# Kernel optimization log

Hardware: AMD Instinct MI355X
Metric: run time of the kernel (lower is better)

Reference implementation:

```python
import jax, jax.numpy as jnp
import numpy as np

N = 50000   # nodes
C = 64      # channels (in == out)
E = 800000  # edges (before self-loops)
EPS = 1e-5  # BatchNorm eps


def _bn(h, gamma, beta):
    # training-mode BatchNorm1d over the node (batch) axis
    mu = h.mean(0)
    var = h.var(0)
    return (h - mu) * jax.lax.rsqrt(var + EPS) * gamma + beta


def setup_inputs() -> dict:
    key = jax.random.key(0)
    ks = jax.random.split(key, 20)
    p = lambda i, shape, s=0.1: jax.random.normal(ks[i], shape, jnp.float32) * s
    src = jax.random.randint(ks[2], (E,), 0, N, dtype=jnp.int32)
    # guarantee no self-loops (PointTransformerConv removes then re-adds them)
    dst = (src + 1 + jax.random.randint(ks[3], (E,), 0, N - 1, dtype=jnp.int32)) % N
    return dict(
        x=p(0, (N, C), 1.0),
        pos=p(1, (N, 3), 1.0),
        edge_index=jnp.stack([src, dst]),
        Win=p(4, (C, C)), bin_=p(5, (C,)), gin=jnp.ones((C,), jnp.float32), betain=jnp.zeros((C,), jnp.float32),
        Wv=p(6, (C, C)), Wk=p(7, (C, C)), Wq=p(8, (C, C)),
        P1=p(9, (3, C)), pb1=p(10, (C,)), P2=p(11, (C, C)), pb2=p(12, (C,)),
        A1=p(13, (C, C)), ab1=p(14, (C,)), A2=p(15, (C, C)), ab2=p(16, (C,)),
        Wout=p(17, (C, C)), bout=p(18, (C,)), gout=jnp.ones((C,), jnp.float32), betaout=jnp.zeros((C,), jnp.float32),
    )


def reference(x, pos, edge_index, Win, bin_, gin, betain, Wv, Wk, Wq,
              P1, pb1, P2, pb2, A1, ab1, A2, ab2, Wout, bout, gout, betaout):
    silu = jax.nn.silu
    # mlp_in: Linear + BN + SiLU (plain_last=False)
    x = silu(_bn(x @ Win + bin_, gin, betain))

    # PointTransformerConv (add_self_loops=True)
    loop = jnp.arange(N, dtype=edge_index.dtype)
    src = jnp.concatenate([edge_index[0], loop])  # j
    dst = jnp.concatenate([edge_index[1], loop])  # i

    v = x @ Wv       # lin (values), bias=False
    k = x @ Wk       # lin_src
    q = x @ Wq       # lin_dst

    # per-edge positional encoding: pos_nn = SiLU(SiLU((pos_i - pos_j) P1 + b) P2 + b)
    delta = silu(silu((pos[dst] - pos[src]) @ P1 + pb1) @ P2 + pb2)  # [Etot, C]
    # attention logits: attn_nn(alpha_i - alpha_j + delta)
    alpha = q[dst] - k[src] + delta
    alpha = silu(silu(alpha @ A1 + ab1) @ A2 + ab2)

    # segment-wise (per-dst-node, per-channel) softmax over neighborhoods
    m = jax.ops.segment_max(alpha, dst, num_segments=N)
    ex = jnp.exp(alpha - m[dst])
    denom = jax.ops.segment_sum(ex, dst, num_segments=N)
    attn = ex / denom[dst]

    # weighted scatter-reduce of messages
    out = jax.ops.segment_sum(attn * (v[src] + delta), dst, num_segments=N)  # [N, C]

    # mlp_out: Linear + BN, act=None
    return _bn(out @ Wout + bout, gout, betaout)
```

## Files before the change

### kernel.cpp

```cpp
#include <hip/hip_runtime.h>

#define CH 64
#define BN_EPS 1e-5f

typedef __attribute__((ext_vector_type(8))) __bf16 bf16x8;
typedef __attribute__((ext_vector_type(4))) __bf16 bf16x4;
typedef __attribute__((ext_vector_type(4))) float f32x4;

__device__ __forceinline__ float silu_f(float x) { return x / (1.0f + __expf(-x)); }

__global__ __launch_bounds__(256) void k_lin_in(
    const float* __restrict__ x, const float* __restrict__ Win, const float* __restrict__ bin,
    float* __restrict__ h, float* __restrict__ ssum, float* __restrict__ ssq, int N)
{
    __shared__ float xt[64 * 64];
    __shared__ float Wl[64 * 64];
    __shared__ float red[2][4][64];
    const int t = threadIdx.x, c = t & 63, g = t >> 6;
    const int row0 = blockIdx.x * 64;

    for (int i = t; i < 64 * 64; i += 256) {
        int r = i >> 6, cc = i & 63;
        int gr = row0 + r;
        xt[i] = (gr < N) ? x[(size_t)gr * CH + cc] : 0.0f;
        Wl[i] = Win[i];
    }
    __syncthreads();

    float acc[16];
    const float b = bin[c];
#pragma unroll
    for (int i = 0; i < 16; ++i) acc[i] = b;
    for (int k = 0; k < 64; ++k) {
        float w = Wl[k * 64 + c];
#pragma unroll
        for (int i = 0; i < 16; ++i) acc[i] += xt[(g * 16 + i) * 64 + k] * w;
    }
    float s = 0.0f, ss = 0.0f;
#pragma unroll
    for (int i = 0; i < 16; ++i) {
        int gr = row0 + g * 16 + i;
        if (gr < N) {
            h[(size_t)gr * CH + c] = acc[i];
            s += acc[i];
            ss += acc[i] * acc[i];
        }
    }
    red[0][g][c] = s;
    red[1][g][c] = ss;
    __syncthreads();
    if (g == 0) {
        atomicAdd(&ssum[c], red[0][0][c] + red[0][1][c] + red[0][2][c] + red[0][3][c]);
        atomicAdd(&ssq[c],  red[1][0][c] + red[1][1][c] + red[1][2][c] + red[1][3][c]);
    }
}

__global__ void k_stats(const float* __restrict__ ssum, const float* __restrict__ ssq,
                        const float* __restrict__ gamma, const float* __restrict__ beta,
                        float* __restrict__ scale, float* __restrict__ shift, int N)
{
    int c = threadIdx.x;
    float inv = 1.0f / (float)N;
    float mu = ssum[c] * inv;
    float var = ssq[c] * inv - mu * mu;
    float sc = gamma[c] * rsqrtf(var + BN_EPS);
    scale[c] = sc;
    shift[c] = beta[c] - mu * sc;
}

__global__ __launch_bounds__(256) void k_vkq(
    const float* __restrict__ h, const float* __restrict__ scale, const float* __restrict__ shift,
    const float* __restrict__ Wv, const float* __restrict__ Wk, const float* __restrict__ Wq,
    __bf16* __restrict__ vv, __bf16* __restrict__ kk, __bf16* __restrict__ qq, int N)
{
    __shared__ float xt[64 * 64];
    __shared__ float Wl[2][64 * 64];
    const int t = threadIdx.x, c = t & 63, g = t >> 6;
    const int row0 = blockIdx.x * 64;

    for (int i = t; i < 64 * 64; i += 256) {
        int r = i >> 6, cc = i & 63;
        int gr = row0 + r;
        float hv = (gr < N) ? h[(size_t)gr * CH + cc] : 0.0f;
        xt[i] = silu_f(hv * scale[cc] + shift[cc]);
        Wl[0][i] = Wv[i];
        Wl[1][i] = Wk[i];
    }
    __syncthreads();

    for (int m = 0; m < 2; ++m) {
        float acc[16];
#pragma unroll
        for (int i = 0; i < 16; ++i) acc[i] = 0.0f;
        for (int k = 0; k < 64; ++k) {
            float w = Wl[m][k * 64 + c];
#pragma unroll
            for (int i = 0; i < 16; ++i) acc[i] += xt[(g * 16 + i) * 64 + k] * w;
        }
        __bf16* o = (m == 0) ? vv : kk;
#pragma unroll
        for (int i = 0; i < 16; ++i) {
            int gr = row0 + g * 16 + i;
            if (gr < N) o[(size_t)gr * CH + c] = (__bf16)acc[i];
        }
    }
    __syncthreads();
    for (int i = t; i < 64 * 64; i += 256) Wl[0][i] = Wq[i];
    __syncthreads();
    {
        float acc[16];
#pragma unroll
        for (int i = 0; i < 16; ++i) acc[i] = 0.0f;
        for (int k = 0; k < 64; ++k) {
            float w = Wl[0][k * 64 + c];
#pragma unroll
            for (int i = 0; i < 16; ++i) acc[i] += xt[(g * 16 + i) * 64 + k] * w;
        }
#pragma unroll
        for (int i = 0; i < 16; ++i) {
            int gr = row0 + g * 16 + i;
            if (gr < N) qq[(size_t)gr * CH + c] = (__bf16)acc[i];
        }
    }
}

__global__ __launch_bounds__(256, 2) void k_edge_mfma(
    const int* __restrict__ srcA, const int* __restrict__ dstA,
    const float* __restrict__ pos,
    const __bf16* __restrict__ vvb, const __bf16* __restrict__ kkb, const __bf16* __restrict__ qqb,
    const float* __restrict__ P1, const float* __restrict__ pb1,
    const float* __restrict__ P2, const float* __restrict__ pb2,
    const float* __restrict__ A1, const float* __restrict__ ab1,
    const float* __restrict__ A2, const float* __restrict__ ab2,
    float* __restrict__ num, float* __restrict__ den,
    int E, int Etot, int nChunks)
{
    __shared__ __align__(16) __bf16 Wtab[3][8][64][8];
    __shared__ __align__(16) __bf16 tb[4][16][66];
    __shared__ __align__(16) __bf16 P1L[3][64];
    __shared__ __align__(16) float pb1L[64];

    const int t = threadIdx.x;
    for (int i = t; i < 3 * 4096; i += 256) {
        int mat = i >> 12, r = i & 4095;
        int j = r & 7, lane = (r >> 3) & 63, ksnt = r >> 9;
        int ks = ksnt & 1, nt = ksnt >> 1;
        int k = ks * 32 + ((lane >> 4) & 3) * 8 + j;
        int n = nt * 16 + (lane & 15);
        const float* W = (mat == 0) ? P2 : ((mat == 1) ? A1 : A2);
        Wtab[mat][ksnt][lane][j] = (__bf16)W[k * 64 + n];
    }
    if (t < 192) P1L[t / 64][t & 63] = (__bf16)P1[t];
    if (t < 64)  pb1L[t] = pb1[t];
    __syncthreads();

    const int l = t & 63, wid = t >> 6, lg = l >> 4, lm = l & 15;
    __bf16* tbw = &tb[wid][0][0];

    float pb2r[4], ab1r[4], ab2r[4];
#pragma unroll
    for (int nt = 0; nt < 4; ++nt) {
        int co = nt * 16 + lm;
        pb2r[nt] = pb2[co];
        ab1r[nt] = ab1[co]; ab2r[nt] = ab2[co];
    }

    const int stride = gridDim.x;
    int ch = blockIdx.x;
    if (ch >= nChunks) return;

    int sC = 0, dC = 0;
    {
        int eA = ch * 64 + wid * 16 + lm;
        if (eA < Etot) { if (eA < E) { sC = srcA[eA]; dC = dstA[eA]; } else { sC = dC = eA - E; } }
    }
    float pdl0, pdl1, pdl2;
    bf16x8 qmk0, qmk1;
    {
        const float* ps = pos + (size_t)sC * 3;
        const float* pd = pos + (size_t)dC * 3;
        pdl0 = pd[0] - ps[0]; pdl1 = pd[1] - ps[1]; pdl2 = pd[2] - ps[2];
        const __bf16* qp = qqb + (size_t)dC * 64 + lg * 8;
        const __bf16* kp = kkb + (size_t)sC * 64 + lg * 8;
        bf16x8 q0 = *(const bf16x8*)qp, q1 = *(const bf16x8*)(qp + 32);
        bf16x8 k0 = *(const bf16x8*)kp, k1 = *(const bf16x8*)(kp + 32);
#pragma unroll
        for (int j = 0; j < 8; ++j) {
            qmk0[j] = (__bf16)((float)q0[j] - (float)k0[j]);
            qmk1[j] = (__bf16)((float)q1[j] - (float)k1[j]);
        }
    }
    __bf16 vcur[4][4];
#pragma unroll
    for (int jj = 0; jj < 4; ++jj) {
        int sD = __shfl(sC, lg * 4 + jj);
        const __bf16* vp = vvb + (size_t)sD * 64 + lm;
#pragma unroll
        for (int nt = 0; nt < 4; ++nt) vcur[jj][nt] = vp[nt * 16];
    }
    int chn = ch + stride;
    bool hn = chn < nChunks;
    int sN = 0, dN = 0;
    if (hn) {
        int eA = chn * 64 + wid * 16 + lm;
        if (eA < Etot) { if (eA < E) { sN = srcA[eA]; dN = dstA[eA]; } else { sN = dN = eA - E; } }
    }

    for (;;) {
        const int e0 = ch * 64 + wid * 16;

        bf16x8 aX0, aX1;
#pragma unroll
        for (int f = 0; f < 2; ++f) {
            const int k0 = f * 32 + lg * 8;
            bf16x8 w0 = *(const bf16x8*)&P1L[0][k0];
            bf16x8 w1 = *(const bf16x8*)&P1L[1][k0];
            bf16x8 w2 = *(const bf16x8*)&P1L[2][k0];
            f32x4 b0 = *(const f32x4*)&pb1L[k0];
            f32x4 b1 = *(const f32x4*)&pb1L[k0 + 4];
#pragma unroll
            for (int j = 0; j < 8; ++j) {
                float bb = (j < 4) ? b0[j & 3] : b1[j & 3];
                float tv = silu_f(pdl0 * (float)w0[j] + pdl1 * (float)w1[j] +
                                  pdl2 * (float)w2[j] + bb);
                if (f == 0) aX0[j] = (__bf16)tv; else aX1[j] = (__bf16)tv;
            }
        }

        f32x4 acc[4];
#pragma unroll
        for (int nt = 0; nt < 4; ++nt) {
            f32x4 a; a[0] = a[1] = a[2] = a[3] = pb2r[nt];
            a = __builtin_amdgcn_mfma_f32_16x16x32_bf16(aX0, *(const bf16x8*)&Wtab[0][nt * 2 + 0][l][0], a, 0, 0, 0);
            a = __builtin_amdgcn_mfma_f32_16x16x32_bf16(aX1, *(const bf16x8*)&Wtab[0][nt * 2 + 1][l][0], a, 0, 0, 0);
            acc[nt] = a;
        }
        bf16x4 dltb[4];
#pragma unroll
        for (int nt = 0; nt < 4; ++nt)
#pragma unroll
            for (int jj = 0; jj < 4; ++jj) {
                float dv = silu_f(acc[nt][jj]);
                dltb[nt][jj] = (__bf16)dv;
                tbw[(lg * 4 + jj) * 66 + nt * 16 + lm] = (__bf16)dv;
            }

        float pdlN0 = 0.f, pdlN1 = 0.f, pdlN2 = 0.f;
        bf16x8 qmkN0, qmkN1;
        __bf16 vN[4][4];
        if (hn) {
            const float* ps = pos + (size_t)sN * 3;
            const float* pd = pos + (size_t)dN * 3;
            pdlN0 = pd[0] - ps[0]; pdlN1 = pd[1] - ps[1]; pdlN2 = pd[2] - ps[2];
            const __bf16* qp = qqb + (size_t)dN * 64 + lg * 8;
            const __bf16* kp = kkb + (size_t)sN * 64 + lg * 8;
            bf16x8 q0 = *(const bf16x8*)qp, q1 = *(const bf16x8*)(qp + 32);
            bf16x8 k0 = *(const bf16x8*)kp, k1 = *(const bf16x8*)(kp + 32);
#pragma unroll
            for (int j = 0; j < 8; ++j) {
                qmkN0[j] = (__bf16)((float)q0[j] - (float)k0[j]);
                qmkN1[j] = (__bf16)((float)q1[j] - (float)k1[j]);
            }
#pragma unroll
            for (int jj = 0; jj < 4; ++jj) {
                int sD = __shfl(sN, lg * 4 + jj);
                const __bf16* vp = vvb + (size_t)sD * 64 + lm;
#pragma unroll
                for (int nt = 0; nt < 4; ++nt) vN[jj][nt] = vp[nt * 16];
            }
        }

        const int chn2 = chn + stride;
        const bool hn2 = hn && (chn2 < nChunks);
        int sNN = 0, dNN = 0;
        if (hn2) {
            int eA = chn2 * 64 + wid * 16 + lm;
            if (eA < Etot) { if (eA < E) { sNN = srcA[eA]; dNN = dstA[eA]; } else { sNN = dNN = eA - E; } }
        }

        bf16x8 dA0 = *(const bf16x8*)&tbw[lm * 66 + lg * 8];
        bf16x8 dA1 = *(const bf16x8*)&tbw[lm * 66 + 32 + lg * 8];
        bf16x8 aA0, aA1;
#pragma unroll
        for (int j = 0; j < 8; ++j) {
            aA0[j] = (__bf16)((float)qmk0[j] + (float)dA0[j]);
            aA1[j] = (__bf16)((float)qmk1[j] + (float)dA1[j]);
        }

#pragma unroll
        for (int nt = 0; nt < 4; ++nt) {
            f32x4 a; a[0] = a[1] = a[2] = a[3] = ab1r[nt];
            a = __builtin_amdgcn_mfma_f32_16x16x32_bf16(aA0, *(const bf16x8*)&Wtab[1][nt * 2 + 0][l][0], a, 0, 0, 0);
            a = __builtin_amdgcn_mfma_f32_16x16x32_bf16(aA1, *(const bf16x8*)&Wtab[1][nt * 2 + 1][l][0], a, 0, 0, 0);
            acc[nt] = a;
        }
#pragma unroll
        for (int nt = 0; nt < 4; ++nt)
#pragma unroll
            for (int jj = 0; jj < 4; ++jj)
                tbw[(lg * 4 + jj) * 66 + nt * 16 + lm] = (__bf16)silu_f(acc[nt][jj]);
        bf16x8 aY0 = *(const bf16x8*)&tbw[lm * 66 + lg * 8];
        bf16x8 aY1 = *(const bf16x8*)&tbw[lm * 66 + 32 + lg * 8];

#pragma unroll
        for (int nt = 0; nt < 4; ++nt) {
            f32x4 a; a[0] = a[1] = a[2] = a[3] = ab2r[nt];
            a = __builtin_amdgcn_mfma_f32_16x16x32_bf16(aY0, *(const bf16x8*)&Wtab[2][nt * 2 + 0][l][0], a, 0, 0, 0);
            a = __builtin_amdgcn_mfma_f32_16x16x32_bf16(aY1, *(const bf16x8*)&Wtab[2][nt * 2 + 1][l][0], a, 0, 0, 0);
            acc[nt] = a;
        }

#pragma unroll
        for (int jj = 0; jj < 4; ++jj) {
            const int eD = e0 + lg * 4 + jj;
            const bool v = eD < Etot;
            const int dD = __shfl(dC, lg * 4 + jj);
            const size_t ob = (size_t)dD * 64 + lm;
#pragma unroll
            for (int nt = 0; nt < 4; ++nt) {
                float ex = v ? __expf(silu_f(acc[nt][jj])) : 0.0f;
                atomicAdd(&den[ob + nt * 16], ex);
                atomicAdd(&num[ob + nt * 16], ex * ((float)vcur[jj][nt] + (float)dltb[nt][jj]));
            }
        }

        if (!hn) break;
        ch = chn; chn = chn2; hn = hn2;
        sC = sN; dC = dN; sN = sNN; dN = dNN;
        pdl0 = pdlN0; pdl1 = pdlN1; pdl2 = pdlN2;
        qmk0 = qmkN0; qmk1 = qmkN1;
#pragma unroll
        for (int jj = 0; jj < 4; ++jj)
#pragma unroll
            for (int nt = 0; nt < 4; ++nt) vcur[jj][nt] = vN[jj][nt];
    }
}

__global__ __launch_bounds__(256) void k_out(
    const float* __restrict__ num, const float* __restrict__ den,
    const float* __restrict__ Wout, const float* __restrict__ bout,
    float* __restrict__ o, float* __restrict__ ssum, float* __restrict__ ssq, int N)
{
    __shared__ float xt[64 * 64];
    __shared__ float Wl[64 * 64];
    __shared__ float red[2][4][64];
    const int t = threadIdx.x, c = t & 63, g = t >> 6;
    const int row0 = blockIdx.x * 64;

    for (int i = t; i < 64 * 64; i += 256) {
        int r = i >> 6, cc = i & 63;
        int gr = row0 + r;
        xt[i] = (gr < N) ? num[(size_t)gr * CH + cc] / den[(size_t)gr * CH + cc] : 0.0f;
        Wl[i] = Wout[i];
    }
    __syncthreads();

    float acc[16];
    const float b = bout[c];
#pragma unroll
    for (int i = 0; i < 16; ++i) acc[i] = b;
    for (int k = 0; k < 64; ++k) {
        float w = Wl[k * 64 + c];
#pragma unroll
        for (int i = 0; i < 16; ++i) acc[i] += xt[(g * 16 + i) * 64 + k] * w;
    }
    float s = 0.0f, ss = 0.0f;
#pragma unroll
    for (int i = 0; i < 16; ++i) {
        int gr = row0 + g * 16 + i;
        if (gr < N) {
            o[(size_t)gr * CH + c] = acc[i];
            s += acc[i];
            ss += acc[i] * acc[i];
        }
    }
    red[0][g][c] = s;
    red[1][g][c] = ss;
    __syncthreads();
    if (g == 0) {
        atomicAdd(&ssum[c], red[0][0][c] + red[0][1][c] + red[0][2][c] + red[0][3][c]);
        atomicAdd(&ssq[c],  red[1][0][c] + red[1][1][c] + red[1][2][c] + red[1][3][c]);
    }
}

__global__ void k_final(const float* __restrict__ o, const float* __restrict__ scale,
                        const float* __restrict__ shift, float* __restrict__ out, int total)
{
    int i = blockIdx.x * blockDim.x + threadIdx.x;
    if (i < total) {
        int c = i & 63;
        out[i] = o[i] * scale[c] + shift[c];
    }
}

extern "C" void kernel_launch(void* const* d_in, const int* in_sizes, int n_in,
                              void* d_out, int out_size, void* d_ws, size_t ws_size,
                              hipStream_t stream)
{
    const float* x      = (const float*)d_in[0];
    const float* pos    = (const float*)d_in[1];
    const int*   ei     = (const int*)d_in[2];
    const float* Win    = (const float*)d_in[3];
    const float* bin    = (const float*)d_in[4];
    const float* gin    = (const float*)d_in[5];
    const float* betain = (const float*)d_in[6];
    const float* Wv     = (const float*)d_in[7];
    const float* Wk     = (const float*)d_in[8];
    const float* Wq     = (const float*)d_in[9];
    const float* P1     = (const float*)d_in[10];
    const float* pb1    = (const float*)d_in[11];
    const float* P2     = (const float*)d_in[12];
    const float* pb2    = (const float*)d_in[13];
    const float* A1     = (const float*)d_in[14];
    const float* ab1    = (const float*)d_in[15];
    const float* A2     = (const float*)d_in[16];
    const float* ab2    = (const float*)d_in[17];
    const float* Wout   = (const float*)d_in[18];
    const float* bout   = (const float*)d_in[19];
    const float* gout   = (const float*)d_in[20];
    const float* betaout= (const float*)d_in[21];

    const int N = in_sizes[0] / CH;
    const int E = in_sizes[2] / 2;
    const int Etot = E + N;
    const int* srcA = ei;
    const int* dstA = ei + E;

    float* ws = (float*)d_ws;
    const size_t NC = (size_t)N * CH;
    float* h    = ws;
    float* num  = h + NC;
    float* den  = num + NC;
    float* st   = den + NC;
    __bf16* vvb = (__bf16*)(st + 512);
    __bf16* kkb = vvb + NC;
    __bf16* qqb = kkb + NC;

    hipMemsetAsync(num, 0, (2 * NC + 512) * sizeof(float), stream);

    const int nb = (N + 63) / 64;
    k_lin_in<<<nb, 256, 0, stream>>>(x, Win, bin, h, st, st + 64, N);
    k_stats<<<1, 64, 0, stream>>>(st, st + 64, gin, betain, st + 128, st + 192, N);
    k_vkq<<<nb, 256, 0, stream>>>(h, st + 128, st + 192, Wv, Wk, Wq, vvb, kkb, qqb, N);

    const int nChunks = (Etot + 63) / 64;
    const int grid = (nChunks < 1024) ? nChunks : 1024;
    k_edge_mfma<<<grid, 256, 0, stream>>>(srcA, dstA, pos, vvb, kkb, qqb,
                                          P1, pb1, P2, pb2, A1, ab1, A2, ab2,
                                          num, den, E, Etot, nChunks);

    k_out<<<nb, 256, 0, stream>>>(num, den, Wout, bout, h, st + 256, st + 320, N);
    k_stats<<<1, 64, 0, stream>>>(st + 256, st + 320, gout, betaout, st + 384, st + 448, N);
    k_final<<<(int)((NC + 255) / 256), 256, 0, stream>>>(h, st + 384, st + 448,
                                                         (float*)d_out, (int)NC);
}
```

Measured before the change: 565.9 us.

## Sort edges by destination (CSR) and reduce per-node in shared memory

Builds a CSR ordering of edges by destination each call, using a histogram, a three-stage scan and an atomic scatter. The edge kernel then assigns 8 destination nodes per block, accumulates softmax numerator and denominator with shared-memory atomics, and writes the normalized result directly. This removes the global float atomics on num/den and the separate division, but adds several sorting kernels and drops the software prefetch pipeline along with the persistent grid. Blocks that get many edges become load-imbalanced, and launching roughly 6250 blocks means reloading the weight tables into shared memory in every block.

```diff
diff --git a/kernel.cpp b/kernel.cpp
--- a/kernel.cpp
+++ b/kernel.cpp
@@ -2,6 +2,7 @@
 
 #define CH 64
 #define BN_EPS 1e-5f
+#define DPB 8
 
 typedef __attribute__((ext_vector_type(8))) __bf16 bf16x8;
 typedef __attribute__((ext_vector_type(4))) __bf16 bf16x4;
@@ -124,21 +125,97 @@
     }
 }
 
-__global__ __launch_bounds__(256, 2) void k_edge_mfma(
-    const int* __restrict__ srcA, const int* __restrict__ dstA,
+__global__ void k_hist(const int* __restrict__ dstA, int* __restrict__ cnt, int E, int Etot)
+{
+    int e = blockIdx.x * blockDim.x + threadIdx.x;
+    if (e < Etot) {
+        int d = (e < E) ? dstA[e] : (e - E);
+        atomicAdd(&cnt[d], 1);
+    }
+}
+
+__global__ __launch_bounds__(256) void k_scan_a(
+    const int* __restrict__ cnt, int* __restrict__ exc, int* __restrict__ bsum, int N)
+{
+    __shared__ int sh[256];
+    const int b = blockIdx.x, t = threadIdx.x;
+    const int base = b * 1024 + t * 4;
+    int v0 = (base + 0 < N) ? cnt[base + 0] : 0;
+    int v1 = (base + 1 < N) ? cnt[base + 1] : 0;
+    int v2 = (base + 2 < N) ? cnt[base + 2] : 0;
+    int v3 = (base + 3 < N) ? cnt[base + 3] : 0;
+    int s = v0 + v1 + v2 + v3;
+    sh[t] = s;
+    __syncthreads();
+    for (int off = 1; off < 256; off <<= 1) {
+        int x = (t >= off) ? sh[t - off] : 0;
+        __syncthreads();
+        sh[t] += x;
+        __syncthreads();
+    }
+    int p = sh[t] - s;
+    if (t == 255) bsum[b] = sh[255];
+    if (base + 0 < N) exc[base + 0] = p; p += v0;
+    if (base + 1 < N) exc[base + 1] = p; p += v1;
+    if (base + 2 < N) exc[base + 2] = p; p += v2;
+    if (base + 3 < N) exc[base + 3] = p;
+}
+
+__global__ __launch_bounds__(256) void k_scan_b(int* __restrict__ bsum, int nb)
+{
+    __shared__ int sh[256];
+    const int t = threadIdx.x;
+    int v = (t < nb) ? bsum[t] : 0;
+    sh[t] = v;
+    __syncthreads();
+    for (int off = 1; off < 256; off <<= 1) {
+        int x = (t >= off) ? sh[t - off] : 0;
+        __syncthreads();
+        sh[t] += x;
+        __syncthreads();
+    }
+    if (t < nb) bsum[t] = sh[t] - v;
+}
+
+__global__ void k_scan_c(const int* __restrict__ exc, const int* __restrict__ bsum,
+                         int* __restrict__ rowptr, int* __restrict__ cur, int N)
+{
+    int i = blockIdx.x * blockDim.x + threadIdx.x;
+    if (i < N) {
+        int r = exc[i] + bsum[i >> 10];
+        rowptr[i] = r;
+        cur[i] = r;
+    }
+}
+
+__global__ void k_scatter(const int* __restrict__ srcA, const int* __restrict__ dstA,
+                          int* __restrict__ cur, int2* __restrict__ sortedSD, int E, int Etot)
+{
+    int e = blockIdx.x * blockDim.x + threadIdx.x;
+    if (e < Etot) {
+        int d, s;
+        if (e < E) { d = dstA[e]; s = srcA[e]; }
+        else       { d = s = e - E; }
+        int p = atomicAdd(&cur[d], 1);
+        sortedSD[p] = make_int2(s, d);
+    }
+}
+
+__global__ __launch_bounds__(256) void k_edge_grp(
+    const int2* __restrict__ sortedSD, const int* __restrict__ rowptr,
     const float* __restrict__ pos,
     const __bf16* __restrict__ vvb, const __bf16* __restrict__ kkb, const __bf16* __restrict__ qqb,
     const float* __restrict__ P1, const float* __restrict__ pb1,
     const float* __restrict__ P2, const float* __restrict__ pb2,
     const float* __restrict__ A1, const float* __restrict__ ab1,
     const float* __restrict__ A2, const float* __restrict__ ab2,
-    float* __restrict__ num, float* __restrict__ den,
-    int E, int Etot, int nChunks)
+    float* __restrict__ pre, int N, int Etot)
 {
     __shared__ __align__(16) __bf16 Wtab[3][8][64][8];
     __shared__ __align__(16) __bf16 tb[4][16][66];
     __shared__ __align__(16) __bf16 P1L[3][64];
     __shared__ __align__(16) float pb1L[64];
+    __shared__ float accS[2][DPB][64];
 
     const int t = threadIdx.x;
     for (int i = t; i < 3 * 4096; i += 256) {
@@ -152,6 +229,8 @@
     }
     if (t < 192) P1L[t / 64][t & 63] = (__bf16)P1[t];
     if (t < 64)  pb1L[t] = pb1[t];
+#pragma unroll
+    for (int i = t; i < 2 * DPB * 64; i += 256) ((float*)accS)[i] = 0.0f;
     __syncthreads();
 
     const int l = t & 63, wid = t >> 6, lg = l >> 4, lm = l & 15;
@@ -165,59 +244,55 @@
         ab1r[nt] = ab1[co]; ab2r[nt] = ab2[co];
     }
 
-    const int stride = gridDim.x;
-    int ch = blockIdx.x;
-    if (ch >= nChunks) return;
-
-    int sC = 0, dC = 0;
-    {
-        int eA = ch * 64 + wid * 16 + lm;
-        if (eA < Etot) { if (eA < E) { sC = srcA[eA]; dC = dstA[eA]; } else { sC = dC = eA - E; } }
-    }
-    float pdl0, pdl1, pdl2;
-    bf16x8 qmk0, qmk1;
-    {
+    const int D0 = blockIdx.x * DPB;
+    const int R0 = rowptr[D0];
+    const int R1 = (D0 + DPB >= N) ? Etot : rowptr[D0 + DPB];
+    const int nE = R1 - R0;
+
+    for (int win = wid; win * 16 < nE; win += 4) {
+        const int eBase = R0 + win * 16;
+        const int eA = eBase + lm;
+        int sC = 0, dloc = 0;
+        int dC = D0;
+        if (eA < R1) {
+            int2 sd = sortedSD[eA];
+            sC = sd.x; dC = sd.y;
+            dloc = dC - D0;
+        }
+
         const float* ps = pos + (size_t)sC * 3;
         const float* pd = pos + (size_t)dC * 3;
-        pdl0 = pd[0] - ps[0]; pdl1 = pd[1] - ps[1]; pdl2 = pd[2] - ps[2];
+        float pdl0 = pd[0] - ps[0], pdl1 = pd[1] - ps[1], pdl2 = pd[2] - ps[2];
         const __bf16* qp = qqb + (size_t)dC * 64 + lg * 8;
         const __bf16* kp = kkb + (size_t)sC * 64 + lg * 8;
         bf16x8 q0 = *(const bf16x8*)qp, q1 = *(const bf16x8*)(qp + 32);
         bf16x8 k0 = *(const bf16x8*)kp, k1 = *(const bf16x8*)(kp + 32);
+        bf16x8 qmk0, qmk1;
 #pragma unroll
         for (int j = 0; j < 8; ++j) {
             qmk0[j] = (__bf16)((float)q0[j] - (float)k0[j]);
             qmk1[j] = (__bf16)((float)q1[j] - (float)k1[j]);
         }
-    }
-    __bf16 vcur[4][4];
-#pragma unroll
-    for (int jj = 0; jj < 4; ++jj) {
-        int sD = __shfl(sC, lg * 4 + jj);
-        const __bf16* vp = vvb + (size_t)sD * 64 + lm;
-#pragma unroll
-        for (int nt = 0; nt < 4; ++nt) vcur[jj][nt] = vp[nt * 16];
-    }
-    int chn = ch + stride;
-    bool hn = chn < nChunks;
-    int sN = 0, dN = 0;
-    if (hn) {
-        int eA = chn * 64 + wid * 16 + lm;
-        if (eA < Etot) { if (eA < E) { sN = srcA[eA]; dN = dstA[eA]; } else { sN = dN = eA - E; } }
-    }
-
-    for (;;) {
-        const int e0 = ch * 64 + wid * 16;
+        int dlocD[4];
+        __bf16 vcur[4][4];
+#pragma unroll
+        for (int jj = 0; jj < 4; ++jj) {
+            int sD = __shfl(sC, lg * 4 + jj);
+            dlocD[jj] = __shfl(dloc, lg * 4 + jj);
+            const __bf16* vp = vvb + (size_t)sD * 64 + lm;
+#pragma unroll
+            for (int nt = 0; nt < 4; ++nt) vcur[jj][nt] = vp[nt * 16];
+        }
 
         bf16x8 aX0, aX1;
 #pragma unroll
         for (int f = 0; f < 2; ++f) {
-            const int k0 = f * 32 + lg * 8;
-            bf16x8 w0 = *(const bf16x8*)&P1L[0][k0];
-            bf16x8 w1 = *(const bf16x8*)&P1L[1][k0];
-            bf16x8 w2 = *(const bf16x8*)&P1L[2][k0];
-            f32x4 b0 = *(const f32x4*)&pb1L[k0];
-            f32x4 b1 = *(const f32x4*)&pb1L[k0 + 4];
+            const int k0i = f * 32 + lg * 8;
+            bf16x8 w0 = *(const bf16x8*)&P1L[0][k0i];
+            bf16x8 w1 = *(const bf16x8*)&P1L[1][k0i];
+            bf16x8 w2 = *(const bf16x8*)&P1L[2][k0i];
+            f32x4 b0 = *(const f32x4*)&pb1L[k0i];
+            f32x4 b1 = *(const f32x4*)&pb1L[k0i + 4];
 #pragma unroll
             for (int j = 0; j < 8; ++j) {
                 float bb = (j < 4) ? b0[j & 3] : b1[j & 3];
@@ -245,39 +320,6 @@
                 tbw[(lg * 4 + jj) * 66 + nt * 16 + lm] = (__bf16)dv;
             }
 
-        float pdlN0 = 0.f, pdlN1 = 0.f, pdlN2 = 0.f;
-        bf16x8 qmkN0, qmkN1;
-        __bf16 vN[4][4];
-        if (hn) {
-            const float* ps = pos + (size_t)sN * 3;
-            const float* pd = pos + (size_t)dN * 3;
-            pdlN0 = pd[0] - ps[0]; pdlN1 = pd[1] - ps[1]; pdlN2 = pd[2] - ps[2];
-            const __bf16* qp = qqb + (size_t)dN * 64 + lg * 8;
-            const __bf16* kp = kkb + (size_t)sN * 64 + lg * 8;
-            bf16x8 q0 = *(const bf16x8*)qp, q1 = *(const bf16x8*)(qp + 32);
-            bf16x8 k0 = *(const bf16x8*)kp, k1 = *(const bf16x8*)(kp + 32);
-#pragma unroll
-            for (int j = 0; j < 8; ++j) {
-                qmkN0[j] = (__bf16)((float)q0[j] - (float)k0[j]);
-                qmkN1[j] = (__bf16)((float)q1[j] - (float)k1[j]);
-            }
-#pragma unroll
-            for (int jj = 0; jj < 4; ++jj) {
-                int sD = __shfl(sN, lg * 4 + jj);
-                const __bf16* vp = vvb + (size_t)sD * 64 + lm;
-#pragma unroll
-                for (int nt = 0; nt < 4; ++nt) vN[jj][nt] = vp[nt * 16];
-            }
-        }
-
-        const int chn2 = chn + stride;
-        const bool hn2 = hn && (chn2 < nChunks);
-        int sNN = 0, dNN = 0;
-        if (hn2) {
-            int eA = chn2 * 64 + wid * 16 + lm;
-            if (eA < Etot) { if (eA < E) { sNN = srcA[eA]; dNN = dstA[eA]; } else { sNN = dNN = eA - E; } }
-        }
-
         bf16x8 dA0 = *(const bf16x8*)&tbw[lm * 66 + lg * 8];
         bf16x8 dA1 = *(const bf16x8*)&tbw[lm * 66 + 32 + lg * 8];
         bf16x8 aA0, aA1;
@@ -312,32 +354,32 @@
 
 #pragma unroll
         for (int jj = 0; jj < 4; ++jj) {
-            const int eD = e0 + lg * 4 + jj;
-            const bool v = eD < Etot;
-            const int dD = __shfl(dC, lg * 4 + jj);
-            const size_t ob = (size_t)dD * 64 + lm;
+            const bool v = (eBase + lg * 4 + jj) < R1;
+            const int dl = dlocD[jj];
 #pragma unroll
             for (int nt = 0; nt < 4; ++nt) {
                 float ex = v ? __expf(silu_f(acc[nt][jj])) : 0.0f;
-                atomicAdd(&den[ob + nt * 16], ex);
-                atomicAdd(&num[ob + nt * 16], ex * ((float)vcur[jj][nt] + (float)dltb[nt][jj]));
+                atomicAdd(&accS[0][dl][nt * 16 + lm], ex);
+                atomicAdd(&accS[1][dl][nt * 16 + lm], ex * ((float)vcur[jj][nt] + (float)dltb[nt][jj]));
             }
         }
-
-        if (!hn) break;
-        ch = chn; chn = chn2; hn = hn2;
-        sC = sN; dC = dN; sN = sNN; dN = dNN;
-        pdl0 = pdlN0; pdl1 = pdlN1; pdl2 = pdlN2;
-        qmk0 = qmkN0; qmk1 = qmkN1;
-#pragma unroll
-        for (int jj = 0; jj < 4; ++jj)
-#pragma unroll
-            for (int nt = 0; nt < 4; ++nt) vcur[jj][nt] = vN[jj][nt];
+    }
+
+    __syncthreads();
+#pragma unroll
+    for (int idx = t; idx < DPB * 64; idx += 256) {
+        int dl = idx >> 6, ch = idx & 63;
+        int node = D0 + dl;
+        if (node < N) {
+            float den = accS[0][dl][ch];
+            float num = accS[1][dl][ch];
+            pre[(size_t)node * 64 + ch] = num / den;
+        }
     }
 }
 
 __global__ __launch_bounds__(256) void k_out(
-    const float* __restrict__ num, const float* __restrict__ den,
+    const float* __restrict__ pre,
     const float* __restrict__ Wout, const float* __restrict__ bout,
     float* __restrict__ o, float* __restrict__ ssum, float* __restrict__ ssq, int N)
 {
@@ -350,7 +392,7 @@
     for (int i = t; i < 64 * 64; i += 256) {
         int r = i >> 6, cc = i & 63;
         int gr = row0 + r;
-        xt[i] = (gr < N) ? num[(size_t)gr * CH + cc] / den[(size_t)gr * CH + cc] : 0.0f;
+        xt[i] = (gr < N) ? pre[(size_t)gr * CH + cc] : 0.0f;
         Wl[i] = Wout[i];
     }
     __syncthreads();
@@ -428,28 +470,39 @@
 
     float* ws = (float*)d_ws;
     const size_t NC = (size_t)N * CH;
-    float* h    = ws;
-    float* num  = h + NC;
-    float* den  = num + NC;
-    float* st   = den + NC;
-    __bf16* vvb = (__bf16*)(st + 512);
+    float* h      = ws;
+    float* pre    = h + NC;
+    float* st     = pre + NC;
+    int*   cnt    = (int*)(st + 512);
+    int*   exc    = cnt + N;
+    int*   rowptr = exc + N;
+    int*   cur    = rowptr + N;
+    int*   bsum   = cur + N;
+    int2*  sortedSD = (int2*)(bsum + 256);
+    __bf16* vvb = (__bf16*)(sortedSD + Etot);
     __bf16* kkb = vvb + NC;
     __bf16* qqb = kkb + NC;
 
-    hipMemsetAsync(num, 0, (2 * NC + 512) * sizeof(float), stream);
+    hipMemsetAsync(st, 0, (512 + (size_t)N) * sizeof(float), stream);
+
+    const int nbScan = (N + 1023) / 1024;
+    k_hist<<<(Etot + 255) / 256, 256, 0, stream>>>(dstA, cnt, E, Etot);
+    k_scan_a<<<nbScan, 256, 0, stream>>>(cnt, exc, bsum, N);
+    k_scan_b<<<1, 256, 0, stream>>>(bsum, nbScan);
+    k_scan_c<<<(N + 255) / 256, 256, 0, stream>>>(exc, bsum, rowptr, cur, N);
+    k_scatter<<<(Etot + 255) / 256, 256, 0, stream>>>(srcA, dstA, cur, sortedSD, E, Etot);
 
     const int nb = (N + 63) / 64;
     k_lin_in<<<nb, 256, 0, stream>>>(x, Win, bin, h, st, st + 64, N);
     k_stats<<<1, 64, 0, stream>>>(st, st + 64, gin, betain, st + 128, st + 192, N);
     k_vkq<<<nb, 256, 0, stream>>>(h, st + 128, st + 192, Wv, Wk, Wq, vvb, kkb, qqb, N);
 
-    const int nChunks = (Etot + 63) / 64;
-    const int grid = (nChunks < 1024) ? nChunks : 1024;
-    k_edge_mfma<<<grid, 256, 0, stream>>>(srcA, dstA, pos, vvb, kkb, qqb,
-                                          P1, pb1, P2, pb2, A1, ab1, A2, ab2,
-                                          num, den, E, Etot, nChunks);
-
-    k_out<<<nb, 256, 0, stream>>>(num, den, Wout, bout, h, st + 256, st + 320, N);
+    const int nBlk = (N + DPB - 1) / DPB;
+    k_edge_grp<<<nBlk, 256, 0, stream>>>(sortedSD, rowptr, pos, vvb, kkb, qqb,
+                                         P1, pb1, P2, pb2, A1, ab1, A2, ab2,
+                                         pre, N, Etot);
+
+    k_out<<<nb, 256, 0, stream>>>(pre, Wout, bout, h, st + 256, st + 320, N);
     k_stats<<<1, 64, 0, stream>>>(st + 256, st + 320, gout, betaout, st + 384, st + 448, N);
     k_final<<<(int)((NC + 255) / 256), 256, 0, stream>>>(h, st + 384, st + 448,
                                                          (float*)d_out, (int)NC);
```

New measurement: 1.107 ms. 95.7% more time.

## Pad positions to float4, drop v-prefetch, double edge-kernel grid

Applied to the files above, without the earlier changes.

A new small kernel copies pos into a padded float4 array, so each edge endpoint's position is read with one vector load instead of three scalar loads. The software prefetch of v rows for the next chunk is removed; v is now loaded at the start of each iteration, which lowers register pressure. The launch-bounds occupancy hint is dropped and the persistent grid is raised from 1024 to 2048 blocks, so more waves are resident to hide gather latency. The trade-off is that v-load latency is no longer covered by prefetch, and there is one extra small kernel launch.

```diff
diff --git a/kernel.cpp b/kernel.cpp
--- a/kernel.cpp
+++ b/kernel.cpp
@@ -68,6 +68,12 @@
     shift[c] = beta[c] - mu * sc;
 }
 
+__global__ void k_pos4(const float* __restrict__ pos, float4* __restrict__ pos4, int N)
+{
+    int i = blockIdx.x * blockDim.x + threadIdx.x;
+    if (i < N) pos4[i] = make_float4(pos[3 * i], pos[3 * i + 1], pos[3 * i + 2], 0.0f);
+}
+
 __global__ __launch_bounds__(256) void k_vkq(
     const float* __restrict__ h, const float* __restrict__ scale, const float* __restrict__ shift,
     const float* __restrict__ Wv, const float* __restrict__ Wk, const float* __restrict__ Wq,
@@ -124,9 +130,9 @@
     }
 }
 
-__global__ __launch_bounds__(256, 2) void k_edge_mfma(
+__global__ __launch_bounds__(256) void k_edge_mfma(
     const int* __restrict__ srcA, const int* __restrict__ dstA,
-    const float* __restrict__ pos,
+    const float4* __restrict__ pos4,
     const __bf16* __restrict__ vvb, const __bf16* __restrict__ kkb, const __bf16* __restrict__ qqb,
     const float* __restrict__ P1, const float* __restrict__ pb1,
     const float* __restrict__ P2, const float* __restrict__ pb2,
@@ -177,9 +183,8 @@
     float pdl0, pdl1, pdl2;
     bf16x8 qmk0, qmk1;
     {
-        const float* ps = pos + (size_t)sC * 3;
-        const float* pd = pos + (size_t)dC * 3;
-        pdl0 = pd[0] - ps[0]; pdl1 = pd[1] - ps[1]; pdl2 = pd[2] - ps[2];
+        float4 ps4 = pos4[sC], pd4 = pos4[dC];
+        pdl0 = pd4.x - ps4.x; pdl1 = pd4.y - ps4.y; pdl2 = pd4.z - ps4.z;
         const __bf16* qp = qqb + (size_t)dC * 64 + lg * 8;
         const __bf16* kp = kkb + (size_t)sC * 64 + lg * 8;
         bf16x8 q0 = *(const bf16x8*)qp, q1 = *(const bf16x8*)(qp + 32);
@@ -189,14 +194,6 @@
             qmk0[j] = (__bf16)((float)q0[j] - (float)k0[j]);
             qmk1[j] = (__bf16)((float)q1[j] - (float)k1[j]);
         }
-    }
-    __bf16 vcur[4][4];
-#pragma unroll
-    for (int jj = 0; jj < 4; ++jj) {
-        int sD = __shfl(sC, lg * 4 + jj);
-        const __bf16* vp = vvb + (size_t)sD * 64 + lm;
-#pragma unroll
-        for (int nt = 0; nt < 4; ++nt) vcur[jj][nt] = vp[nt * 16];
     }
     int chn = ch + stride;
     bool hn = chn < nChunks;
@@ -209,15 +206,26 @@
     for (;;) {
         const int e0 = ch * 64 + wid * 16;
 
+        int dD[4];
+        __bf16 vcur[4][4];
+#pragma unroll
+        for (int jj = 0; jj < 4; ++jj) {
+            int sD = __shfl(sC, lg * 4 + jj);
+            dD[jj] = __shfl(dC, lg * 4 + jj);
+            const __bf16* vp = vvb + (size_t)sD * 64 + lm;
+#pragma unroll
+            for (int nt = 0; nt < 4; ++nt) vcur[jj][nt] = vp[nt * 16];
+        }
+
         bf16x8 aX0, aX1;
 #pragma unroll
         for (int f = 0; f < 2; ++f) {
-            const int k0 = f * 32 + lg * 8;
-            bf16x8 w0 = *(const bf16x8*)&P1L[0][k0];
-            bf16x8 w1 = *(const bf16x8*)&P1L[1][k0];
-            bf16x8 w2 = *(const bf16x8*)&P1L[2][k0];
-            f32x4 b0 = *(const f32x4*)&pb1L[k0];
-            f32x4 b1 = *(const f32x4*)&pb1L[k0 + 4];
+            const int k0i = f * 32 + lg * 8;
+            bf16x8 w0 = *(const bf16x8*)&P1L[0][k0i];
+            bf16x8 w1 = *(const bf16x8*)&P1L[1][k0i];
+            bf16x8 w2 = *(const bf16x8*)&P1L[2][k0i];
+            f32x4 b0 = *(const f32x4*)&pb1L[k0i];
+            f32x4 b1 = *(const f32x4*)&pb1L[k0i + 4];
 #pragma unroll
             for (int j = 0; j < 8; ++j) {
                 float bb = (j < 4) ? b0[j & 3] : b1[j & 3];
@@ -247,11 +255,9 @@
 
         float pdlN0 = 0.f, pdlN1 = 0.f, pdlN2 = 0.f;
         bf16x8 qmkN0, qmkN1;
-        __bf16 vN[4][4];
         if (hn) {
-            const float* ps = pos + (size_t)sN * 3;
-            const float* pd = pos + (size_t)dN * 3;
-            pdlN0 = pd[0] - ps[0]; pdlN1 = pd[1] - ps[1]; pdlN2 = pd[2] - ps[2];
+            float4 ps4 = pos4[sN], pd4 = pos4[dN];
+            pdlN0 = pd4.x - ps4.x; pdlN1 = pd4.y - ps4.y; pdlN2 = pd4.z - ps4.z;
             const __bf16* qp = qqb + (size_t)dN * 64 + lg * 8;
             const __bf16* kp = kkb + (size_t)sN * 64 + lg * 8;
             bf16x8 q0 = *(const bf16x8*)qp, q1 = *(const bf16x8*)(qp + 32);
@@ -260,13 +266,6 @@
             for (int j = 0; j < 8; ++j) {
                 qmkN0[j] = (__bf16)((float)q0[j] - (float)k0[j]);
                 qmkN1[j] = (__bf16)((float)q1[j] - (float)k1[j]);
-            }
-#pragma unroll
-            for (int jj = 0; jj < 4; ++jj) {
-                int sD = __shfl(sN, lg * 4 + jj);
-                const __bf16* vp = vvb + (size_t)sD * 64 + lm;
-#pragma unroll
-                for (int nt = 0; nt < 4; ++nt) vN[jj][nt] = vp[nt * 16];
             }
         }
 
@@ -314,8 +313,7 @@
         for (int jj = 0; jj < 4; ++jj) {
             const int eD = e0 + lg * 4 + jj;
             const bool v = eD < Etot;
-            const int dD = __shfl(dC, lg * 4 + jj);
-            const size_t ob = (size_t)dD * 64 + lm;
+            const size_t ob = (size_t)dD[jj] * 64 + lm;
 #pragma unroll
             for (int nt = 0; nt < 4; ++nt) {
                 float ex = v ? __expf(silu_f(acc[nt][jj])) : 0.0f;
@@ -329,10 +327,6 @@
         sC = sN; dC = dN; sN = sNN; dN = dNN;
         pdl0 = pdlN0; pdl1 = pdlN1; pdl2 = pdlN2;
         qmk0 = qmkN0; qmk1 = qmkN1;
-#pragma unroll
-        for (int jj = 0; jj < 4; ++jj)
-#pragma unroll
-            for (int nt = 0; nt < 4; ++nt) vcur[jj][nt] = vN[jj][nt];
     }
 }
 
@@ -428,24 +422,26 @@
 
     float* ws = (float*)d_ws;
     const size_t NC = (size_t)N * CH;
-    float* h    = ws;
-    float* num  = h + NC;
-    float* den  = num + NC;
-    float* st   = den + NC;
-    __bf16* vvb = (__bf16*)(st + 512);
-    __bf16* kkb = vvb + NC;
-    __bf16* qqb = kkb + NC;
+    float* h     = ws;
+    float* num   = h + NC;
+    float* den   = num + NC;
+    float* st    = den + NC;
+    float4* pos4 = (float4*)(st + 512);
+    __bf16* vvb  = (__bf16*)(pos4 + N);
+    __bf16* kkb  = vvb + NC;
+    __bf16* qqb  = kkb + NC;
 
     hipMemsetAsync(num, 0, (2 * NC + 512) * sizeof(float), stream);
 
     const int nb = (N + 63) / 64;
+    k_pos4<<<(N + 255) / 256, 256, 0, stream>>>(pos, pos4, N);
     k_lin_in<<<nb, 256, 0, stream>>>(x, Win, bin, h, st, st + 64, N);
     k_stats<<<1, 64, 0, stream>>>(st, st + 64, gin, betain, st + 128, st + 192, N);
     k_vkq<<<nb, 256, 0, stream>>>(h, st + 128, st + 192, Wv, Wk, Wq, vvb, kkb, qqb, N);
 
     const int nChunks = (Etot + 63) / 64;
-    const int grid = (nChunks < 1024) ? nChunks : 1024;
-    k_edge_mfma<<<grid, 256, 0, stream>>>(srcA, dstA, pos, vvb, kkb, qqb,
+    const int grid = (nChunks < 2048) ? nChunks : 2048;
+    k_edge_mfma<<<grid, 256, 0, stream>>>(srcA, dstA, pos4, vvb, kkb, qqb,
                                           P1, pb1, P2, pb2, A1, ab1, A2, ab2,
                                           num, den, E, Etot, nChunks);
 
```

New measurement: 523.3 us. -7.5%, faster.
